# Kernel tuning notes

Hardware: AMD Instinct MI355X
Metric: run time of the kernel (lower is better)

Reference implementation:

```python
import jax, jax.numpy as jnp
import numpy as np

N, D, DB, E, H = 1024, 512, 64, 32768, 1024

def setup_inputs() -> dict:
    key = jax.random.key(0)
    k = jax.random.split(key, 6)
    object_feats = jax.random.normal(k[0], (N, D), dtype=jnp.float32)
    bboxes_embedding = jax.random.normal(k[1], (N, N, DB), dtype=jnp.float32)
    pairs = jax.random.randint(k[2], (E, 2), 0, N, dtype=jnp.int64)
    # Kaiming-normal-ish init for the two Linear layers
    W1 = jax.random.normal(k[3], (D + D + DB, H), dtype=jnp.float32) * np.sqrt(2.0 / (D + D + DB))
    b1 = jnp.zeros((H,), dtype=jnp.float32)
    W2 = jax.random.normal(k[4], (H, D), dtype=jnp.float32) * np.sqrt(2.0 / H)
    b2 = jnp.zeros((D,), dtype=jnp.float32)
    return {"object_feats": object_feats, "bboxes_embedding": bboxes_embedding,
            "pairs": pairs, "W1": W1, "b1": b1, "W2": W2, "b2": b2}

def reference(object_feats, bboxes_embedding, pairs, W1, b1, W2, b2):
    sub = pairs[:, 0]
    obj = pairs[:, 1]
    # gather pair features: [E, D] each, plus pairwise bbox embedding [E, DB]
    f_sub = object_feats[sub]
    f_obj = object_feats[obj]
    bb = bboxes_embedding[sub, obj]
    x = jnp.concatenate((f_sub, f_obj, bb), axis=1)  # [E, 2D+DB]
    h = jax.nn.relu(x @ W1 + b1)
    out = h @ W2 + b2  # [E, D]
    n = object_feats.shape[0]
    # scatter-mean into subject nodes; each node's own feature is included once,
    # so new_feat[i] = (object_feats[i] + sum_{pairs with sub==i} out) / (1 + count[i]).
    # Nodes with no incident pairs keep their original feature (count==0 -> identity).
    seg_sum = jax.ops.segment_sum(out, sub, num_segments=n)  # [N, D]
    count = jax.ops.segment_sum(jnp.ones((out.shape[0],), dtype=out.dtype), sub, num_segments=n)
    new_feats = (object_feats + seg_sum) / (1.0 + count)[:, None]
    return (new_feats, bboxes_embedding, pairs)
```

## Files before the change

### kernel.cpp

```cpp
#include <hip/hip_runtime.h>

#define N_OBJ 1024
#define E_P   32768

typedef float f32x4 __attribute__((ext_vector_type(4)));
typedef short bf16x8 __attribute__((ext_vector_type(8)));
typedef unsigned short u16x4 __attribute__((ext_vector_type(4)));

__device__ __forceinline__ unsigned short f2bf(float f) {
    unsigned u = __float_as_uint(f);
    u = u + 0x7FFFu + ((u >> 16) & 1u);
    return (unsigned short)(u >> 16);
}

#define OFF_A    0
#define LEN_A    3670016
#define OFF_B    (OFF_A + LEN_A)
#define LEN_B    4194304
#define OFF_SEG  (OFF_B + LEN_B)
#define LEN_SEG  4194304
#define OFF_OUT  (OFF_SEG + LEN_SEG)
#define LEN_OUT  4718592

__device__ __forceinline__ void copy_role(const float4* __restrict__ src,
                                          float4* __restrict__ dst,
                                          int off, int len, int nb, int cb) {
    int stride = nb * 256;
    int i = off + cb * 256 + threadIdx.x;
    int end = off + len;
    for (; i + stride < end; i += 2 * stride) {
        float4 a = src[i];
        float4 b = src[i + stride];
        dst[i] = a;
        dst[i + stride] = b;
    }
    if (i < end) dst[i] = src[i];
}

__global__ __launch_bounds__(256) void k_a(const float* __restrict__ W1,
                                           const float* __restrict__ W2,
                                           const float* __restrict__ feats,
                                           const int* __restrict__ pairs,
                                           unsigned short* __restrict__ w1pqT,
                                           unsigned short* __restrict__ w1cT,
                                           unsigned short* __restrict__ w2T,
                                           unsigned short* __restrict__ featsb,
                                           float* __restrict__ out_pairs,
                                           int* __restrict__ counts,
                                           int* __restrict__ rank,
                                           const float4* __restrict__ csrc,
                                           float4* __restrict__ cdst) {
    int bid = blockIdx.x, tid = threadIdx.x;
    if ((bid % 3) == 2) { copy_role(csrc, cdst, OFF_A, LEN_A, 1056, bid / 3); return; }
    int job = (bid / 3) * 2 + (bid % 3);
    if (job >= 1856) {
        int i = (job - 1856) * 256 + tid;
        out_pairs[i] = (float)pairs[i];
        if (i < E_P) rank[i] = atomicAdd(&counts[pairs[2 * i]], 1);
        return;
    }
    if (job >= 1600) {
        int base = (job - 1600) * 2048 + tid * 8;
        float4 v0 = *(const float4*)&feats[base];
        float4 v1 = *(const float4*)&feats[base + 4];
        u16x4 o0 = { f2bf(v0.x), f2bf(v0.y), f2bf(v0.z), f2bf(v0.w) };
        u16x4 o1 = { f2bf(v1.x), f2bf(v1.y), f2bf(v1.z), f2bf(v1.w) };
        *(u16x4*)&featsb[base] = o0;
        *(u16x4*)&featsb[base + 4] = o1;
        return;
    }
    const float* in; unsigned short* out;
    int LDI, LDO, r0, c0, nbase, kbase;
    if (job < 1024) {
        r0 = (job >> 5) * 32; c0 = (job & 31) * 32;
        in = W1; LDI = 1024; out = w1pqT; LDO = 512;
        nbase = c0 + (r0 >= 512 ? 1024 : 0); kbase = r0 & 511;
    } else if (job < 1088) {
        int t = job - 1024; r0 = 1024 + (t >> 5) * 32; c0 = (t & 31) * 32;
        in = W1; LDI = 1024; out = w1cT; LDO = 64;
        nbase = c0; kbase = r0 - 1024;
    } else {
        int t = job - 1088; r0 = (t >> 4) * 32; c0 = (t & 15) * 32;
        in = W2; LDI = 512; out = w2T; LDO = 1024;
        nbase = c0; kbase = r0;
    }
    __shared__ float lds[32][33];
    int ti = tid >> 3, tj = (tid & 7) * 4;
    float4 v = *(const float4*)&in[(size_t)(r0 + ti) * LDI + c0 + tj];
    lds[ti][tj] = v.x; lds[ti][tj + 1] = v.y; lds[ti][tj + 2] = v.z; lds[ti][tj + 3] = v.w;
    __syncthreads();
    int oc = tid >> 3, oj = (tid & 7) * 4;
    u16x4 o = { f2bf(lds[oj][oc]), f2bf(lds[oj + 1][oc]),
                f2bf(lds[oj + 2][oc]), f2bf(lds[oj + 3][oc]) };
    *(u16x4*)&out[(size_t)(nbase + oc) * LDO + kbase + oj] = o;
}

__global__ __launch_bounds__(256) void k_b(const int* __restrict__ counts,
                                           const int* __restrict__ rank,
                                           const int* __restrict__ pairs,
                                           int* __restrict__ csr_obj,
                                           unsigned* __restrict__ brec,
                                           int* __restrict__ bcnt,
                                           const unsigned short* __restrict__ featsb,
                                           const unsigned short* __restrict__ w1pqT,
                                           const float* __restrict__ b1,
                                           float* __restrict__ P, float* __restrict__ Q,
                                           const float4* __restrict__ csrc,
                                           float4* __restrict__ cdst) {
    int bid = blockIdx.x, tid = threadIdx.x;
    if ((bid % 3) < 2) { copy_role(csrc, cdst, OFF_B, LEN_B, 1282, (bid / 3) * 2 + (bid % 3)); return; }
    int role = bid / 3;

    if (role >= 129) {
        int job = role - 129;
        int m0 = (job >> 5) * 64, n0 = (job & 31) * 64;
        int w = tid >> 6, l = tid & 63;
        int ln = l & 15, kb = (l >> 4) * 8;
        int row = m0 + w * 16 + ln;
        f32x4 acc[4] = {};
        for (int k0 = 0; k0 < 512; k0 += 32) {
            bf16x8 a = *(const bf16x8*)&featsb[(size_t)row * 512 + k0 + kb];
            #pragma unroll
            for (int f = 0; f < 4; ++f) {
                bf16x8 b = *(const bf16x8*)&w1pqT[(size_t)(n0 + f * 16 + ln) * 512 + k0 + kb];
                acc[f] = __builtin_amdgcn_mfma_f32_16x16x32_bf16(a, b, acc[f], 0, 0, 0);
            }
        }
        int mr = m0 + w * 16 + (l >> 4) * 4;
        if (n0 < 1024) {
            #pragma unroll
            for (int f = 0; f < 4; ++f) {
                int n = n0 + f * 16 + ln;
                float b1v = b1[n];
                #pragma unroll
                for (int r = 0; r < 4; ++r)
                    P[(size_t)(mr + r) * 1024 + n] = acc[f][r] + b1v;
            }
        } else {
            #pragma unroll
            for (int f = 0; f < 4; ++f) {
                int n = n0 - 1024 + f * 16 + ln;
                #pragma unroll
                for (int r = 0; r < 4; ++r)
                    Q[(size_t)(mr + r) * 1024 + n] = acc[f][r];
            }
        }
        return;
    }

    __shared__ int sbuf[2][256];
    __shared__ int soff[1024];
    int c[4]; int s = 0;
    #pragma unroll
    for (int i = 0; i < 4; ++i) { c[i] = counts[tid * 4 + i]; s += c[i]; }
    sbuf[0][tid] = s;
    __syncthreads();
    int sel = 0;
    for (int d = 1; d < 256; d <<= 1) {
        int v = sbuf[sel][tid];
        if (tid >= d) v += sbuf[sel][tid - d];
        sbuf[sel ^ 1][tid] = v;
        sel ^= 1;
        __syncthreads();
    }
    int base = sbuf[sel][tid] - s;
    int run = base;
    #pragma unroll
    for (int i = 0; i < 4; ++i) { soff[tid * 4 + i] = run; run += c[i]; }
    __syncthreads();

    if (role >= 1) {
        int e = (role - 1) * 256 + tid;
        int sub = pairs[2 * e];
        csr_obj[soff[sub] + rank[e]] = pairs[2 * e + 1];
        return;
    }

    int nb[4]; int t = 0;
    #pragma unroll
    for (int i = 0; i < 4; ++i) { nb[i] = (c[i] + 31) >> 5; t += nb[i]; }
    __syncthreads();
    sbuf[0][tid] = t;
    __syncthreads();
    sel = 0;
    for (int d = 1; d < 256; d <<= 1) {
        int v = sbuf[sel][tid];
        if (tid >= d) v += sbuf[sel][tid - d];
        sbuf[sel ^ 1][tid] = v;
        sel ^= 1;
        __syncthreads();
    }
    int bpos = sbuf[sel][tid] - t;
    int run2 = base;
    #pragma unroll
    for (int i = 0; i < 4; ++i) {
        int seg = tid * 4 + i;
        for (int k = 0; k < nb[i]; ++k) {
            int st = run2 + k * 32;
            int cnt = c[i] - k * 32; if (cnt > 32) cnt = 32;
            brec[bpos++] = (unsigned)st | ((unsigned)seg << 16) | ((unsigned)(cnt - 1) << 26);
        }
        run2 += c[i];
    }
    if (tid == 255) bcnt[0] = bpos;
}

__global__ __launch_bounds__(256) void k_seg(const int* __restrict__ csr_obj,
                                             const unsigned* __restrict__ brec,
                                             const int* __restrict__ bcnt,
                                             const float* __restrict__ bb,
                                             const unsigned short* __restrict__ w1cT,
                                             const float* __restrict__ P,
                                             const float* __restrict__ Q,
                                             float* __restrict__ HS,
                                             const float4* __restrict__ csrc,
                                             float4* __restrict__ cdst) {
    int bid = blockIdx.x;
    if ((bid % 5) == 4) { copy_role(csrc, cdst, OFF_SEG, LEN_SEG, 2048, bid / 5); return; }
    int job = (bid / 5) * 4 + (bid % 5);
    int b = job >> 2, qd = job & 3;
    if (b >= bcnt[0]) return;
    unsigned rec = brec[b];
    const int start = rec & 0xFFFF;
    const int seg = (rec >> 16) & 0x3FF;
    const int n = ((rec >> 26) & 31) + 1;

    const int tid = threadIdx.x, w = tid >> 6, l = tid & 63;
    const int ln = l & 15, g4 = l >> 4, kb = g4 * 8;
    const int cbase = qd * 256;
    const int wbase = cbase + w * 64;

    __shared__ float qs[32][256];

    {
        int p = tid >> 3, j = tid & 7;
        int op = csr_obj[start + (p < n ? p : n - 1)];
        const float* qrow = &Q[(size_t)op * 1024 + cbase];
        #pragma unroll
        for (int i = 0; i < 8; ++i) {
            int c = j * 4 + i * 32;
            *(float4*)&qs[p][c] = *(const float4*)&qrow[c];
        }
    }

    const int nA = n < 16 ? n : 16;
    const int nB = n - 16;
    int iA = start + (ln < nA ? ln : nA - 1);
    int iB = (nB > 0) ? (start + 16 + (ln < nB ? ln : nB - 1)) : iA;
    int objA = csr_obj[iA];
    int objB = csr_obj[iB];

    const float* brA = &bb[((size_t)seg * 1024 + (size_t)objA) * 64];
    const float* brB = &bb[((size_t)seg * 1024 + (size_t)objB) * 64];
    float4 a0 = *(const float4*)&brA[kb];
    float4 a1 = *(const float4*)&brA[kb + 4];
    float4 a2 = *(const float4*)&brA[32 + kb];
    float4 a3 = *(const float4*)&brA[32 + kb + 4];
    float4 c0 = *(const float4*)&brB[kb];
    float4 c1 = *(const float4*)&brB[kb + 4];
    float4 c2 = *(const float4*)&brB[32 + kb];
    float4 c3 = *(const float4*)&brB[32 + kb + 4];
    bf16x8 A0a, A1a, A0b, A1b;
    A0a[0] = (short)f2bf(a0.x); A0a[1] = (short)f2bf(a0.y); A0a[2] = (short)f2bf(a0.z); A0a[3] = (short)f2bf(a0.w);
    A0a[4] = (short)f2bf(a1.x); A0a[5] = (short)f2bf(a1.y); A0a[6] = (short)f2bf(a1.z); A0a[7] = (short)f2bf(a1.w);
    A1a[0] = (short)f2bf(a2.x); A1a[1] = (short)f2bf(a2.y); A1a[2] = (short)f2bf(a2.z); A1a[3] = (short)f2bf(a2.w);
    A1a[4] = (short)f2bf(a3.x); A1a[5] = (short)f2bf(a3.y); A1a[6] = (short)f2bf(a3.z); A1a[7] = (short)f2bf(a3.w);
    A0b[0] = (short)f2bf(c0.x); A0b[1] = (short)f2bf(c0.y); A0b[2] = (short)f2bf(c0.z); A0b[3] = (short)f2bf(c0.w);
    A0b[4] = (short)f2bf(c1.x); A0b[5] = (short)f2bf(c1.y); A0b[6] = (short)f2bf(c1.z); A0b[7] = (short)f2bf(c1.w);
    A1b[0] = (short)f2bf(c2.x); A1b[1] = (short)f2bf(c2.y); A1b[2] = (short)f2bf(c2.z); A1b[3] = (short)f2bf(c2.w);
    A1b[4] = (short)f2bf(c3.x); A1b[5] = (short)f2bf(c3.y); A1b[6] = (short)f2bf(c3.z); A1b[7] = (short)f2bf(c3.w);

    bool vA0 = (g4 * 4 + 0) < nA, vA1 = (g4 * 4 + 1) < nA;
    bool vA2 = (g4 * 4 + 2) < nA, vA3 = (g4 * 4 + 3) < nA;
    bool vB0 = (g4 * 4 + 0) < nB, vB1 = (g4 * 4 + 1) < nB;
    bool vB2 = (g4 * 4 + 2) < nB, vB3 = (g4 * 4 + 3) < nB;

    float pv[4];
    #pragma unroll
    for (int f = 0; f < 4; ++f)
        pv[f] = P[(size_t)seg * 1024 + wbase + f * 16 + ln];

    __syncthreads();

    #pragma unroll
    for (int f = 0; f < 4; ++f) {
        int col = wbase + f * 16 + ln;
        int cc = col - cbase;
        const unsigned short* wr = &w1cT[(size_t)col * 64];
        bf16x8 b0 = *(const bf16x8*)&wr[kb];
        bf16x8 b1 = *(const bf16x8*)&wr[32 + kb];
        f32x4 dA = {0.f, 0.f, 0.f, 0.f};
        dA = __builtin_amdgcn_mfma_f32_16x16x32_bf16(A0a, b0, dA, 0, 0, 0);
        dA = __builtin_amdgcn_mfma_f32_16x16x32_bf16(A1a, b1, dA, 0, 0, 0);
        f32x4 dB = {0.f, 0.f, 0.f, 0.f};
        dB = __builtin_amdgcn_mfma_f32_16x16x32_bf16(A0b, b0, dB, 0, 0, 0);
        dB = __builtin_amdgcn_mfma_f32_16x16x32_bf16(A1b, b1, dB, 0, 0, 0);
        float qA0 = qs[g4 * 4 + 0][cc];
        float qA1 = qs[g4 * 4 + 1][cc];
        float qA2 = qs[g4 * 4 + 2][cc];
        float qA3 = qs[g4 * 4 + 3][cc];
        float qB0 = qs[16 + g4 * 4 + 0][cc];
        float qB1 = qs[16 + g4 * 4 + 1][cc];
        float qB2 = qs[16 + g4 * 4 + 2][cc];
        float qB3 = qs[16 + g4 * 4 + 3][cc];
        float h = 0.f;
        h += vA0 ? fmaxf(dA[0] + pv[f] + qA0, 0.f) : 0.f;
        h += vA1 ? fmaxf(dA[1] + pv[f] + qA1, 0.f) : 0.f;
        h += vA2 ? fmaxf(dA[2] + pv[f] + qA2, 0.f) : 0.f;
        h += vA3 ? fmaxf(dA[3] + pv[f] + qA3, 0.f) : 0.f;
        h += vB0 ? fmaxf(dB[0] + pv[f] + qB0, 0.f) : 0.f;
        h += vB1 ? fmaxf(dB[1] + pv[f] + qB1, 0.f) : 0.f;
        h += vB2 ? fmaxf(dB[2] + pv[f] + qB2, 0.f) : 0.f;
        h += vB3 ? fmaxf(dB[3] + pv[f] + qB3, 0.f) : 0.f;
        h += __shfl_xor(h, 16);
        h += __shfl_xor(h, 32);
        if (l < 16) atomicAdd(&HS[(size_t)seg * 1024 + wbase + f * 16 + l], h);
    }
}

__global__ __launch_bounds__(256) void k_out(const float* __restrict__ HS,
                                             const unsigned short* __restrict__ w2T,
                                             const float* __restrict__ feats,
                                             const float* __restrict__ b2,
                                             const int* __restrict__ counts,
                                             float* __restrict__ out0,
                                             const float4* __restrict__ csrc,
                                             float4* __restrict__ cdst) {
    int bid = blockIdx.x;
    if ((bid % 17) != 16) { copy_role(csrc, cdst, OFF_OUT, LEN_OUT, 2048, (bid / 17) * 16 + (bid % 17)); return; }
    int job = bid / 17;
    int m0 = (job >> 3) * 64, n0 = (job & 7) * 64;
    int tid = threadIdx.x, w = tid >> 6, l = tid & 63;
    int ln = l & 15, kb = (l >> 4) * 8;
    int row = m0 + w * 16 + ln;
    f32x4 acc[4] = {};
    for (int k0 = 0; k0 < 1024; k0 += 32) {
        const float* hp = &HS[(size_t)row * 1024 + k0 + kb];
        float4 h0 = *(const float4*)&hp[0];
        float4 h1 = *(const float4*)&hp[4];
        bf16x8 a;
        a[0] = (short)f2bf(h0.x); a[1] = (short)f2bf(h0.y); a[2] = (short)f2bf(h0.z); a[3] = (short)f2bf(h0.w);
        a[4] = (short)f2bf(h1.x); a[5] = (short)f2bf(h1.y); a[6] = (short)f2bf(h1.z); a[7] = (short)f2bf(h1.w);
        #pragma unroll
        for (int f = 0; f < 4; ++f) {
            bf16x8 b = *(const bf16x8*)&w2T[(size_t)(n0 + f * 16 + ln) * 1024 + k0 + kb];
            acc[f] = __builtin_amdgcn_mfma_f32_16x16x32_bf16(a, b, acc[f], 0, 0, 0);
        }
    }
    int mr = m0 + w * 16 + (l >> 4) * 4;
    float cv[4], inv[4];
    #pragma unroll
    for (int r = 0; r < 4; ++r) {
        float c = (float)counts[mr + r];
        cv[r] = c;
        inv[r] = 1.0f / (1.0f + c);
    }
    #pragma unroll
    for (int f = 0; f < 4; ++f) {
        int n = n0 + f * 16 + ln;
        float b2v = b2[n];
        #pragma unroll
        for (int r = 0; r < 4; ++r) {
            float fv = feats[(size_t)(mr + r) * 512 + n];
            out0[(size_t)(mr + r) * 512 + n] = (fv + acc[f][r] + cv[r] * b2v) * inv[r];
        }
    }
}

extern "C" void kernel_launch(void* const* d_in, const int* in_sizes, int n_in,
                              void* d_out, int out_size, void* d_ws, size_t ws_size,
                              hipStream_t stream) {
    const float* feats = (const float*)d_in[0];
    const float* bb    = (const float*)d_in[1];
    const int*   pairs = (const int*)d_in[2];
    const float* W1    = (const float*)d_in[3];
    const float* b1    = (const float*)d_in[4];
    const float* W2    = (const float*)d_in[5];
    const float* b2    = (const float*)d_in[6];

    float* out        = (float*)d_out;
    float* out_feats  = out;
    float* out_bb     = out + (size_t)N_OBJ * 512;
    float* out_pairs  = out + (size_t)N_OBJ * 512 + (size_t)N_OBJ * N_OBJ * 64;

    char* w = (char*)d_ws;
    unsigned short* featsb = (unsigned short*)w;
    unsigned short* w1pqT  = (unsigned short*)(w + (1u << 20));
    float*          HS     = (float*)w;
    unsigned short* w1cT   = (unsigned short*)(w + (4u << 20));
    unsigned short* w2T    = (unsigned short*)(w + (4u << 20) + (128u << 10));
    float* P = (float*)(w + (5u << 20) + (128u << 10));
    float* Q = (float*)(w + (9u << 20) + (128u << 10));
    char* ints = w + (13u << 20) + (128u << 10);
    int*      counts  = (int*)ints;
    int*      csr_obj = (int*)(ints + 4096);
    unsigned* brec    = (unsigned*)(ints + 4096 + 131072);
    int*      bcnt    = (int*)(ints + 4096 + 131072 + 16384);
    int*      rank    = (int*)(ints + 4096 + 131072 + 16384 + 64);

    const float4* cbb  = (const float4*)bb;
    float4*       cobb = (float4*)out_bb;

    hipMemsetAsync(counts, 0, 4096, stream);

    k_a<<<3168, 256, 0, stream>>>(W1, W2, feats, pairs, w1pqT, w1cT, w2T, featsb,
                                  out_pairs, counts, rank, cbb, cobb);
    k_b<<<1923, 256, 0, stream>>>(counts, rank, pairs, csr_obj, brec, bcnt,
                                  featsb, w1pqT, b1, P, Q, cbb, cobb);

    hipMemsetAsync(HS, 0, (size_t)N_OBJ * 1024 * sizeof(float), stream);

    k_seg<<<10240, 256, 0, stream>>>(csr_obj, brec, bcnt, bb, w1cT, P, Q, HS, cbb, cobb);
    k_out<<<2176, 256, 0, stream>>>(HS, w2T, feats, b2, counts, out_feats, cbb, cobb);
}
```

Measured before the change: 231.5 us.

## Move bbox embedding copy out of compute kernels into a dedicated trailing kernel

The 256 MB passthrough copy of the bbox embedding was spread across all four compute kernels as interleaved copy-role blocks. Those blocks are removed, and a standalone copy kernel now runs after the compute kernels. This simplifies block indexing and stops the copy from competing with the compute work. It gives up the overlap of bandwidth-bound copying with the latency-bound compute stages, so the copy time may now simply add to the total.

```diff
diff --git a/kernel.cpp b/kernel.cpp
--- a/kernel.cpp
+++ b/kernel.cpp
@@ -13,28 +13,15 @@
     return (unsigned short)(u >> 16);
 }
 
-#define OFF_A    0
-#define LEN_A    3670016
-#define OFF_B    (OFF_A + LEN_A)
-#define LEN_B    4194304
-#define OFF_SEG  (OFF_B + LEN_B)
-#define LEN_SEG  4194304
-#define OFF_OUT  (OFF_SEG + LEN_SEG)
-#define LEN_OUT  4718592
-
-__device__ __forceinline__ void copy_role(const float4* __restrict__ src,
-                                          float4* __restrict__ dst,
-                                          int off, int len, int nb, int cb) {
-    int stride = nb * 256;
-    int i = off + cb * 256 + threadIdx.x;
-    int end = off + len;
-    for (; i + stride < end; i += 2 * stride) {
-        float4 a = src[i];
-        float4 b = src[i + stride];
-        dst[i] = a;
-        dst[i + stride] = b;
-    }
-    if (i < end) dst[i] = src[i];
+__global__ __launch_bounds__(256) void k_copy(const float4* __restrict__ src,
+                                              float4* __restrict__ dst) {
+    int i = blockIdx.x * 256 + threadIdx.x;
+    const int stride = 8192 * 256;
+    #pragma unroll
+    for (int it = 0; it < 8; ++it) {
+        dst[i] = src[i];
+        i += stride;
+    }
 }
 
 __global__ __launch_bounds__(256) void k_a(const float* __restrict__ W1,
@@ -47,12 +34,8 @@
                                            unsigned short* __restrict__ featsb,
                                            float* __restrict__ out_pairs,
                                            int* __restrict__ counts,
-                                           int* __restrict__ rank,
-                                           const float4* __restrict__ csrc,
-                                           float4* __restrict__ cdst) {
-    int bid = blockIdx.x, tid = threadIdx.x;
-    if ((bid % 3) == 2) { copy_role(csrc, cdst, OFF_A, LEN_A, 1056, bid / 3); return; }
-    int job = (bid / 3) * 2 + (bid % 3);
+                                           int* __restrict__ rank) {
+    int job = blockIdx.x, tid = threadIdx.x;
     if (job >= 1856) {
         int i = (job - 1856) * 256 + tid;
         out_pairs[i] = (float)pairs[i];
@@ -104,12 +87,8 @@
                                            const unsigned short* __restrict__ featsb,
                                            const unsigned short* __restrict__ w1pqT,
                                            const float* __restrict__ b1,
-                                           float* __restrict__ P, float* __restrict__ Q,
-                                           const float4* __restrict__ csrc,
-                                           float4* __restrict__ cdst) {
-    int bid = blockIdx.x, tid = threadIdx.x;
-    if ((bid % 3) < 2) { copy_role(csrc, cdst, OFF_B, LEN_B, 1282, (bid / 3) * 2 + (bid % 3)); return; }
-    int role = bid / 3;
+                                           float* __restrict__ P, float* __restrict__ Q) {
+    int role = blockIdx.x, tid = threadIdx.x;
 
     if (role >= 129) {
         int job = role - 129;
@@ -212,12 +191,8 @@
                                              const unsigned short* __restrict__ w1cT,
                                              const float* __restrict__ P,
                                              const float* __restrict__ Q,
-                                             float* __restrict__ HS,
-                                             const float4* __restrict__ csrc,
-                                             float4* __restrict__ cdst) {
-    int bid = blockIdx.x;
-    if ((bid % 5) == 4) { copy_role(csrc, cdst, OFF_SEG, LEN_SEG, 2048, bid / 5); return; }
-    int job = (bid / 5) * 4 + (bid % 5);
+                                             float* __restrict__ HS) {
+    int job = blockIdx.x;
     int b = job >> 2, qd = job & 3;
     if (b >= bcnt[0]) return;
     unsigned rec = brec[b];
@@ -323,12 +298,8 @@
                                              const float* __restrict__ feats,
                                              const float* __restrict__ b2,
                                              const int* __restrict__ counts,
-                                             float* __restrict__ out0,
-                                             const float4* __restrict__ csrc,
-                                             float4* __restrict__ cdst) {
-    int bid = blockIdx.x;
-    if ((bid % 17) != 16) { copy_role(csrc, cdst, OFF_OUT, LEN_OUT, 2048, (bid / 17) * 16 + (bid % 17)); return; }
-    int job = bid / 17;
+                                             float* __restrict__ out0) {
+    int job = blockIdx.x;
     int m0 = (job >> 3) * 64, n0 = (job & 7) * 64;
     int tid = threadIdx.x, w = tid >> 6, l = tid & 63;
     int ln = l & 15, kb = (l >> 4) * 8;
@@ -398,18 +369,17 @@
     int*      bcnt    = (int*)(ints + 4096 + 131072 + 16384);
     int*      rank    = (int*)(ints + 4096 + 131072 + 16384 + 64);
 
-    const float4* cbb  = (const float4*)bb;
-    float4*       cobb = (float4*)out_bb;
-
     hipMemsetAsync(counts, 0, 4096, stream);
 
-    k_a<<<3168, 256, 0, stream>>>(W1, W2, feats, pairs, w1pqT, w1cT, w2T, featsb,
-                                  out_pairs, counts, rank, cbb, cobb);
-    k_b<<<1923, 256, 0, stream>>>(counts, rank, pairs, csr_obj, brec, bcnt,
-                                  featsb, w1pqT, b1, P, Q, cbb, cobb);
+    k_a<<<2112, 256, 0, stream>>>(W1, W2, feats, pairs, w1pqT, w1cT, w2T, featsb,
+                                  out_pairs, counts, rank);
+    k_b<<<641, 256, 0, stream>>>(counts, rank, pairs, csr_obj, brec, bcnt,
+                                 featsb, w1pqT, b1, P, Q);
 
     hipMemsetAsync(HS, 0, (size_t)N_OBJ * 1024 * sizeof(float), stream);
 
-    k_seg<<<10240, 256, 0, stream>>>(csr_obj, brec, bcnt, bb, w1cT, P, Q, HS, cbb, cobb);
-    k_out<<<2176, 256, 0, stream>>>(HS, w2T, feats, b2, counts, out_feats, cbb, cobb);
-}
+    k_seg<<<8192, 256, 0, stream>>>(csr_obj, brec, bcnt, bb, w1cT, P, Q, HS);
+    k_out<<<128, 256, 0, stream>>>(HS, w2T, feats, b2, counts, out_feats);
+
+    k_copy<<<8192, 256, 0, stream>>>((const float4*)bb, (float4*)out_bb);
+}
```

Measured after the change: 248.5 us. +7.3%, slower.

## Pre-gather pair bbox rows, use nontemporal copies, rebalance copy split across kernels

Applied to the files above, without the earlier changes.

Kernel k_a now gathers the 64-float bbox embedding row for each pair into a contiguous buffer indexed by edge id. k_b records each edge id in CSR order, and k_seg reads this compact buffer instead of scattering into the 256 MB bbox tensor. The pass-through copy of bboxes_embedding now uses nontemporal loads and stores, and its share is moved between kernels, with more in k_seg and less in k_b and k_out. The two memsets become tiny kernels. The gather adds an extra 8 MB write and read in exchange for better locality in k_seg and less cache pollution from the bulk copy.

```diff
diff --git a/kernel.cpp b/kernel.cpp
--- a/kernel.cpp
+++ b/kernel.cpp
@@ -16,31 +16,47 @@
 #define OFF_A    0
 #define LEN_A    3670016
 #define OFF_B    (OFF_A + LEN_A)
-#define LEN_B    4194304
+#define LEN_B    3145728
 #define OFF_SEG  (OFF_B + LEN_B)
-#define LEN_SEG  4194304
+#define LEN_SEG  6815744
 #define OFF_OUT  (OFF_SEG + LEN_SEG)
-#define LEN_OUT  4718592
-
-__device__ __forceinline__ void copy_role(const float4* __restrict__ src,
-                                          float4* __restrict__ dst,
-                                          int off, int len, int nb, int cb) {
+#define LEN_OUT  3145728
+
+__device__ __forceinline__ void copy_nt(const f32x4* __restrict__ src,
+                                        f32x4* __restrict__ dst,
+                                        int off, int len, int nb, int cb) {
     int stride = nb * 256;
     int i = off + cb * 256 + threadIdx.x;
     int end = off + len;
     for (; i + stride < end; i += 2 * stride) {
-        float4 a = src[i];
-        float4 b = src[i + stride];
-        dst[i] = a;
-        dst[i + stride] = b;
-    }
-    if (i < end) dst[i] = src[i];
+        f32x4 a = __builtin_nontemporal_load(&src[i]);
+        f32x4 b = __builtin_nontemporal_load(&src[i + stride]);
+        __builtin_nontemporal_store(a, &dst[i]);
+        __builtin_nontemporal_store(b, &dst[i + stride]);
+    }
+    if (i < end) {
+        f32x4 a = __builtin_nontemporal_load(&src[i]);
+        __builtin_nontemporal_store(a, &dst[i]);
+    }
+}
+
+__global__ __launch_bounds__(256) void k_zero(int* __restrict__ counts) {
+    ((int4*)counts)[threadIdx.x] = make_int4(0, 0, 0, 0);
+}
+
+__global__ __launch_bounds__(256) void k_zero_hs(float4* __restrict__ hs4) {
+    int i = blockIdx.x * 256 + threadIdx.x;
+    const int stride = 256 * 256;
+    float4 z = make_float4(0.f, 0.f, 0.f, 0.f);
+    #pragma unroll
+    for (int it = 0; it < 4; ++it) { hs4[i] = z; i += stride; }
 }
 
 __global__ __launch_bounds__(256) void k_a(const float* __restrict__ W1,
                                            const float* __restrict__ W2,
                                            const float* __restrict__ feats,
                                            const int* __restrict__ pairs,
+                                           const float* __restrict__ bb,
                                            unsigned short* __restrict__ w1pqT,
                                            unsigned short* __restrict__ w1cT,
                                            unsigned short* __restrict__ w2T,
@@ -48,11 +64,25 @@
                                            float* __restrict__ out_pairs,
                                            int* __restrict__ counts,
                                            int* __restrict__ rank,
-                                           const float4* __restrict__ csrc,
-                                           float4* __restrict__ cdst) {
+                                           float* __restrict__ bbg,
+                                           const f32x4* __restrict__ csrc,
+                                           f32x4* __restrict__ cdst) {
     int bid = blockIdx.x, tid = threadIdx.x;
-    if ((bid % 3) == 2) { copy_role(csrc, cdst, OFF_A, LEN_A, 1056, bid / 3); return; }
+    if ((bid % 3) == 2) { copy_nt(csrc, cdst, OFF_A, LEN_A, 1184, bid / 3); return; }
     int job = (bid / 3) * 2 + (bid % 3);
+    if (job >= 2240) return;
+    if (job >= 2112) {
+        int e = (job - 2112) * 256 + tid;
+        int sub = pairs[2 * e], obj = pairs[2 * e + 1];
+        const f32x4* src = (const f32x4*)&bb[((size_t)sub * 1024 + (size_t)obj) * 64];
+        f32x4* dst = (f32x4*)&bbg[(size_t)e * 64];
+        #pragma unroll
+        for (int i = 0; i < 16; ++i) {
+            f32x4 v = __builtin_nontemporal_load(&src[i]);
+            dst[i] = v;
+        }
+        return;
+    }
     if (job >= 1856) {
         int i = (job - 1856) * 256 + tid;
         out_pairs[i] = (float)pairs[i];
@@ -99,16 +129,17 @@
                                            const int* __restrict__ rank,
                                            const int* __restrict__ pairs,
                                            int* __restrict__ csr_obj,
+                                           int* __restrict__ csr_e,
                                            unsigned* __restrict__ brec,
                                            int* __restrict__ bcnt,
                                            const unsigned short* __restrict__ featsb,
                                            const unsigned short* __restrict__ w1pqT,
                                            const float* __restrict__ b1,
                                            float* __restrict__ P, float* __restrict__ Q,
-                                           const float4* __restrict__ csrc,
-                                           float4* __restrict__ cdst) {
+                                           const f32x4* __restrict__ csrc,
+                                           f32x4* __restrict__ cdst) {
     int bid = blockIdx.x, tid = threadIdx.x;
-    if ((bid % 3) < 2) { copy_role(csrc, cdst, OFF_B, LEN_B, 1282, (bid / 3) * 2 + (bid % 3)); return; }
+    if ((bid % 3) < 2) { copy_nt(csrc, cdst, OFF_B, LEN_B, 1282, (bid / 3) * 2 + (bid % 3)); return; }
     int role = bid / 3;
 
     if (role >= 129) {
@@ -172,7 +203,9 @@
     if (role >= 1) {
         int e = (role - 1) * 256 + tid;
         int sub = pairs[2 * e];
-        csr_obj[soff[sub] + rank[e]] = pairs[2 * e + 1];
+        int pos = soff[sub] + rank[e];
+        csr_obj[pos] = pairs[2 * e + 1];
+        csr_e[pos] = e;
         return;
     }
 
@@ -206,17 +239,18 @@
 }
 
 __global__ __launch_bounds__(256) void k_seg(const int* __restrict__ csr_obj,
+                                             const int* __restrict__ csr_e,
                                              const unsigned* __restrict__ brec,
                                              const int* __restrict__ bcnt,
-                                             const float* __restrict__ bb,
+                                             const float* __restrict__ bbg,
                                              const unsigned short* __restrict__ w1cT,
                                              const float* __restrict__ P,
                                              const float* __restrict__ Q,
                                              float* __restrict__ HS,
-                                             const float4* __restrict__ csrc,
-                                             float4* __restrict__ cdst) {
+                                             const f32x4* __restrict__ csrc,
+                                             f32x4* __restrict__ cdst) {
     int bid = blockIdx.x;
-    if ((bid % 5) == 4) { copy_role(csrc, cdst, OFF_SEG, LEN_SEG, 2048, bid / 5); return; }
+    if ((bid % 5) == 4) { copy_nt(csrc, cdst, OFF_SEG, LEN_SEG, 2048, bid / 5); return; }
     int job = (bid / 5) * 4 + (bid % 5);
     int b = job >> 2, qd = job & 3;
     if (b >= bcnt[0]) return;
@@ -247,11 +281,11 @@
     const int nB = n - 16;
     int iA = start + (ln < nA ? ln : nA - 1);
     int iB = (nB > 0) ? (start + 16 + (ln < nB ? ln : nB - 1)) : iA;
-    int objA = csr_obj[iA];
-    int objB = csr_obj[iB];
-
-    const float* brA = &bb[((size_t)seg * 1024 + (size_t)objA) * 64];
-    const float* brB = &bb[((size_t)seg * 1024 + (size_t)objB) * 64];
+    int eA = csr_e[iA];
+    int eB = csr_e[iB];
+
+    const float* brA = &bbg[(size_t)eA * 64];
+    const float* brB = &bbg[(size_t)eB * 64];
     float4 a0 = *(const float4*)&brA[kb];
     float4 a1 = *(const float4*)&brA[kb + 4];
     float4 a2 = *(const float4*)&brA[32 + kb];
@@ -324,10 +358,10 @@
                                              const float* __restrict__ b2,
                                              const int* __restrict__ counts,
                                              float* __restrict__ out0,
-                                             const float4* __restrict__ csrc,
-                                             float4* __restrict__ cdst) {
+                                             const f32x4* __restrict__ csrc,
+                                             f32x4* __restrict__ cdst) {
     int bid = blockIdx.x;
-    if ((bid % 17) != 16) { copy_role(csrc, cdst, OFF_OUT, LEN_OUT, 2048, (bid / 17) * 16 + (bid % 17)); return; }
+    if ((bid % 17) != 16) { copy_nt(csrc, cdst, OFF_OUT, LEN_OUT, 2048, (bid / 17) * 16 + (bid % 17)); return; }
     int job = bid / 17;
     int m0 = (job >> 3) * 64, n0 = (job & 7) * 64;
     int tid = threadIdx.x, w = tid >> 6, l = tid & 63;
@@ -397,19 +431,22 @@
     unsigned* brec    = (unsigned*)(ints + 4096 + 131072);
     int*      bcnt    = (int*)(ints + 4096 + 131072 + 16384);
     int*      rank    = (int*)(ints + 4096 + 131072 + 16384 + 64);
-
-    const float4* cbb  = (const float4*)bb;
-    float4*       cobb = (float4*)out_bb;
-
-    hipMemsetAsync(counts, 0, 4096, stream);
-
-    k_a<<<3168, 256, 0, stream>>>(W1, W2, feats, pairs, w1pqT, w1cT, w2T, featsb,
-                                  out_pairs, counts, rank, cbb, cobb);
-    k_b<<<1923, 256, 0, stream>>>(counts, rank, pairs, csr_obj, brec, bcnt,
+    int*      csr_e   = (int*)(ints + 4096 + 131072 + 16384 + 64 + 131072);
+    float*    bbg     = (float*)(w + (14u << 20));
+
+    const f32x4* cbb  = (const f32x4*)bb;
+    f32x4*       cobb = (f32x4*)out_bb;
+
+    k_zero<<<1, 256, 0, stream>>>(counts);
+
+    k_a<<<3552, 256, 0, stream>>>(W1, W2, feats, pairs, bb, w1pqT, w1cT, w2T, featsb,
+                                  out_pairs, counts, rank, bbg, cbb, cobb);
+    k_b<<<1923, 256, 0, stream>>>(counts, rank, pairs, csr_obj, csr_e, brec, bcnt,
                                   featsb, w1pqT, b1, P, Q, cbb, cobb);
 
-    hipMemsetAsync(HS, 0, (size_t)N_OBJ * 1024 * sizeof(float), stream);
-
-    k_seg<<<10240, 256, 0, stream>>>(csr_obj, brec, bcnt, bb, w1cT, P, Q, HS, cbb, cobb);
+    k_zero_hs<<<256, 256, 0, stream>>>((float4*)HS);
+
+    k_seg<<<10240, 256, 0, stream>>>(csr_obj, csr_e, brec, bcnt, bbg, w1cT, P, Q, HS,
+                                     cbb, cobb);
     k_out<<<2176, 256, 0, stream>>>(HS, w2T, feats, b2, counts, out_feats, cbb, cobb);
 }
```

New measurement: 235.1 us. No clear change (+1.5%).
